# Optimization experiments

Hardware: AMD Instinct MI355X
Metric: run time of the kernel (lower is better)

## Reference

```python
import jax, jax.numpy as jnp
import numpy as np

NUM_DAYS = 4096
NUM_ATTR = 512
MB = 128  # minibatch_size (sliding-window length)
HID = 500


def setup_inputs() -> dict:
    key = jax.random.key(0)
    kx, k1, kb1, k2, kb2 = jax.random.split(key, 5)
    bound1 = 1.0 / np.sqrt(NUM_ATTR)
    bound2 = 1.0 / np.sqrt(HID)
    return {
        "x": jax.random.normal(kx, (NUM_DAYS, NUM_ATTR), dtype=jnp.float32),
        "W1": jax.random.uniform(k1, (NUM_ATTR, HID), jnp.float32, -bound1, bound1),
        "b1": jax.random.uniform(kb1, (HID,), jnp.float32, -bound1, bound1),
        "W2": jax.random.uniform(k2, (HID, 1), jnp.float32, -bound2, bound2),
        "b2": jax.random.uniform(kb2, (1,), jnp.float32, -bound2, bound2),
    }


def reference(x, W1, b1, W2, b2):
    num_days = x.shape[0]
    num_batches = num_days - MB  # number of sliding windows
    # window gather indices: [num_batches, MB]
    idx = jnp.arange(num_batches)[:, None] + jnp.arange(MB)[None, :]
    xw = x[idx]                                   # [num_batches, MB, num_attr]
    h = jnp.einsum('wma,ah->wmh', xw, W1) + b1    # [num_batches, MB, 500]
    out = jnp.einsum('wmh,ho->wmo', h, W2) + b2   # [num_batches, MB, 1]
    # torch loop cats all windows along dim 0 (first window replaces sentinel)
    return out.reshape(num_batches * MB, 1)
```

## Files before the change

### kernel.cpp

```cpp
#include <hip/hip_runtime.h>

#define NUM_DAYS    4096
#define NUM_ATTR    512
#define MB_WIN      128
#define HID         500
#define NUM_BATCHES (NUM_DAYS - MB_WIN)
#define NUM_Y       (NUM_BATCHES + MB_WIN - 1)
#define OUT_ELEMS   (NUM_BATCHES * MB_WIN)

__global__ __launch_bounds__(64) void k_fold_weights(
    const float* __restrict__ W1, const float* __restrict__ b1,
    const float* __restrict__ W2, const float* __restrict__ b2,
    float* __restrict__ v, float* __restrict__ c) {
    const int b    = blockIdx.x;
    const int lane = threadIdx.x;
    const float* src = (b < NUM_ATTR) ? (W1 + (size_t)b * HID) : b1;
    float acc = 0.f;
    const float4* s4 = (const float4*)src;
    const float4* w4 = (const float4*)W2;
    #pragma unroll
    for (int j = lane; j < 125; j += 64) {
        float4 a = s4[j], w = w4[j];
        acc += a.x * w.x + a.y * w.y + a.z * w.z + a.w * w.w;
    }
    #pragma unroll
    for (int off = 32; off >= 1; off >>= 1) acc += __shfl_down(acc, off, 64);
    if (lane == 0) {
        if (b < NUM_ATTR) v[b] = acc;
        else              *c   = acc + b2[0];
    }
}

__global__ __launch_bounds__(64) void k_dot_scatter(
    const float* __restrict__ x, const float* __restrict__ v,
    const float* __restrict__ c, float* __restrict__ out) {
    const int b    = blockIdx.x;
    const int lane = threadIdx.x;
    const int d    = ((b & 15) << 8) | (b >> 4);
    if (d >= NUM_Y) return;

    const float4* xr = (const float4*)(x + (size_t)d * NUM_ATTR);
    const float4* vr = (const float4*)v;
    float4 a0 = xr[lane];
    float4 a1 = xr[lane + 64];
    float4 v0 = vr[lane];
    float4 v1 = vr[lane + 64];
    float acc = a0.x * v0.x + a0.y * v0.y + a0.z * v0.z + a0.w * v0.w
              + a1.x * v1.x + a1.y * v1.y + a1.z * v1.z + a1.w * v1.w;
    #pragma unroll
    for (int off = 32; off >= 1; off >>= 1) acc += __shfl_xor(acc, off, 64);
    const float yv = acc + *c;

    const int m0 = lane,      w0 = d - m0;
    const int m1 = lane + 64, w1 = d - m1;
    if (w0 >= 0 && w0 < NUM_BATCHES) out[(size_t)w0 * MB_WIN + m0] = yv;
    if (w1 >= 0 && w1 < NUM_BATCHES) out[(size_t)w1 * MB_WIN + m1] = yv;
}

extern "C" void kernel_launch(void* const* d_in, const int* in_sizes, int n_in,
                              void* d_out, int out_size, void* d_ws, size_t ws_size,
                              hipStream_t stream) {
    const float* x  = (const float*)d_in[0];
    const float* W1 = (const float*)d_in[1];
    const float* b1 = (const float*)d_in[2];
    const float* W2 = (const float*)d_in[3];
    const float* b2 = (const float*)d_in[4];
    float* out = (float*)d_out;

    float* ws = (float*)d_ws;
    float* v  = ws;
    float* c  = ws + 512;

    k_fold_weights<<<NUM_ATTR + 1, 64, 0, stream>>>(W1, b1, W2, b2, v, c);
    k_dot_scatter<<<NUM_DAYS, 64, 0, stream>>>(x, v, c, out);
}
```

Measured before the change: 69.47 us.

## Split dot-scatter into row dot kernel and coalesced float4 replicate kernel

Splits the fused dot-and-scatter kernel into two. The first computes one scalar per day with four waves per block and writes it to a workspace buffer. The second writes the sliding-window output as contiguous float4 stores that read from the small y buffer. This replaces the strided scattered output writes with fully coalesced vector stores, at the cost of an extra kernel launch and a round trip through the workspace.

```diff
diff --git a/kernel.cpp b/kernel.cpp
--- a/kernel.cpp
+++ b/kernel.cpp
@@ -31,12 +31,12 @@
     }
 }
 
-__global__ __launch_bounds__(64) void k_dot_scatter(
+__global__ __launch_bounds__(256) void k_dot(
     const float* __restrict__ x, const float* __restrict__ v,
-    const float* __restrict__ c, float* __restrict__ out) {
-    const int b    = blockIdx.x;
-    const int lane = threadIdx.x;
-    const int d    = ((b & 15) << 8) | (b >> 4);
+    const float* __restrict__ c, float* __restrict__ y) {
+    const int wv   = threadIdx.x >> 6;
+    const int lane = threadIdx.x & 63;
+    const int d    = (blockIdx.x << 2) | wv;
     if (d >= NUM_Y) return;
 
     const float4* xr = (const float4*)(x + (size_t)d * NUM_ATTR);
@@ -49,12 +49,21 @@
               + a1.x * v1.x + a1.y * v1.y + a1.z * v1.z + a1.w * v1.w;
     #pragma unroll
     for (int off = 32; off >= 1; off >>= 1) acc += __shfl_xor(acc, off, 64);
-    const float yv = acc + *c;
+    if (lane == 0) y[d] = acc + *c;
+}
 
-    const int m0 = lane,      w0 = d - m0;
-    const int m1 = lane + 64, w1 = d - m1;
-    if (w0 >= 0 && w0 < NUM_BATCHES) out[(size_t)w0 * MB_WIN + m0] = yv;
-    if (w1 >= 0 && w1 < NUM_BATCHES) out[(size_t)w1 * MB_WIN + m1] = yv;
+__global__ __launch_bounds__(256) void k_replicate(
+    const float* __restrict__ y, float4* __restrict__ out4) {
+    const int t = blockIdx.x * 256 + threadIdx.x;
+    const int w = t >> 5;
+    const int l = t & 31;
+    const int base = w + (l << 2);
+    float4 r;
+    r.x = y[base + 0];
+    r.y = y[base + 1];
+    r.z = y[base + 2];
+    r.w = y[base + 3];
+    out4[t] = r;
 }
 
 extern "C" void kernel_launch(void* const* d_in, const int* in_sizes, int n_in,
@@ -70,7 +79,9 @@
     float* ws = (float*)d_ws;
     float* v  = ws;
     float* c  = ws + 512;
+    float* y  = ws + 576;
 
     k_fold_weights<<<NUM_ATTR + 1, 64, 0, stream>>>(W1, b1, W2, b2, v, c);
-    k_dot_scatter<<<NUM_DAYS, 64, 0, stream>>>(x, v, c, out);
+    k_dot<<<(NUM_Y + 3) / 4, 256, 0, stream>>>(x, v, c, y);
+    k_replicate<<<(OUT_ELEMS / 4) / 256, 256, 0, stream>>>(y, (float4*)out);
 }
```

Measured after the change: 68.40 us. Within noise of the previous version (-1.5%).

## Compute window dots per output tile in shared memory and write coalesced float4 rows

Applied to the files above, without the earlier changes.

Replaces the per-day dot-and-scatter kernel with one that gives each block 16 output windows. The block recomputes the 143 day dot products those windows need into shared memory, then writes the 16x128 output tile with contiguous float4 stores. This removes the strided scattered writes of the old kernel at the cost of recomputing each x row dot about 9 times, which adds x reads that should mostly hit L2.

```diff
diff --git a/kernel.cpp b/kernel.cpp
--- a/kernel.cpp
+++ b/kernel.cpp
@@ -7,6 +7,9 @@
 #define NUM_BATCHES (NUM_DAYS - MB_WIN)
 #define NUM_Y       (NUM_BATCHES + MB_WIN - 1)
 #define OUT_ELEMS   (NUM_BATCHES * MB_WIN)
+
+#define ROWS_PER_BLK 16
+#define DOTS_PER_BLK (ROWS_PER_BLK + MB_WIN - 1)
 
 __global__ __launch_bounds__(64) void k_fold_weights(
     const float* __restrict__ W1, const float* __restrict__ b1,
@@ -31,30 +34,48 @@
     }
 }
 
-__global__ __launch_bounds__(64) void k_dot_scatter(
+__global__ __launch_bounds__(256) void k_out(
     const float* __restrict__ x, const float* __restrict__ v,
-    const float* __restrict__ c, float* __restrict__ out) {
-    const int b    = blockIdx.x;
-    const int lane = threadIdx.x;
-    const int d    = ((b & 15) << 8) | (b >> 4);
-    if (d >= NUM_Y) return;
+    const float* __restrict__ c, float4* __restrict__ out4) {
+    __shared__ float y_s[DOTS_PER_BLK];
 
-    const float4* xr = (const float4*)(x + (size_t)d * NUM_ATTR);
+    const int wv   = threadIdx.x >> 6;
+    const int lane = threadIdx.x & 63;
+    const int w0   = blockIdx.x * ROWS_PER_BLK;
+
     const float4* vr = (const float4*)v;
-    float4 a0 = xr[lane];
-    float4 a1 = xr[lane + 64];
-    float4 v0 = vr[lane];
-    float4 v1 = vr[lane + 64];
-    float acc = a0.x * v0.x + a0.y * v0.y + a0.z * v0.z + a0.w * v0.w
-              + a1.x * v1.x + a1.y * v1.y + a1.z * v1.z + a1.w * v1.w;
+    const float4  v0 = vr[lane];
+    const float4  v1 = vr[lane + 64];
+    const float   cc = *c;
+
+    for (int i = wv; i < DOTS_PER_BLK; i += 4) {
+        const int d = w0 + i;
+        const float4* xr = (const float4*)(x + (size_t)d * NUM_ATTR);
+        float4 a0 = xr[lane];
+        float4 a1 = xr[lane + 64];
+        float acc = a0.x * v0.x + a0.y * v0.y + a0.z * v0.z + a0.w * v0.w
+                  + a1.x * v1.x + a1.y * v1.y + a1.z * v1.z + a1.w * v1.w;
+        #pragma unroll
+        for (int off = 32; off >= 1; off >>= 1) acc += __shfl_xor(acc, off, 64);
+        if (lane == 0) y_s[i] = acc + cc;
+    }
+
+    __syncthreads();
+
+    const int base4 = w0 * (MB_WIN / 4);
     #pragma unroll
-    for (int off = 32; off >= 1; off >>= 1) acc += __shfl_xor(acc, off, 64);
-    const float yv = acc + *c;
-
-    const int m0 = lane,      w0 = d - m0;
-    const int m1 = lane + 64, w1 = d - m1;
-    if (w0 >= 0 && w0 < NUM_BATCHES) out[(size_t)w0 * MB_WIN + m0] = yv;
-    if (w1 >= 0 && w1 < NUM_BATCHES) out[(size_t)w1 * MB_WIN + m1] = yv;
+    for (int k = 0; k < 2; ++k) {
+        const int t = threadIdx.x + k * 256;
+        const int r = t >> 5;
+        const int l = t & 31;
+        const int s = r + (l << 2);
+        float4 o;
+        o.x = y_s[s + 0];
+        o.y = y_s[s + 1];
+        o.z = y_s[s + 2];
+        o.w = y_s[s + 3];
+        out4[base4 + t] = o;
+    }
 }
 
 extern "C" void kernel_launch(void* const* d_in, const int* in_sizes, int n_in,
@@ -65,12 +86,12 @@
     const float* b1 = (const float*)d_in[2];
     const float* W2 = (const float*)d_in[3];
     const float* b2 = (const float*)d_in[4];
-    float* out = (float*)d_out;
+    float4* out = (float4*)d_out;
 
     float* ws = (float*)d_ws;
     float* v  = ws;
     float* c  = ws + 512;
 
     k_fold_weights<<<NUM_ATTR + 1, 64, 0, stream>>>(W1, b1, W2, b2, v, c);
-    k_dot_scatter<<<NUM_DAYS, 64, 0, stream>>>(x, v, c, out);
+    k_out<<<NUM_BATCHES / ROWS_PER_BLK, 256, 0, stream>>>(x, v, c, out);
 }
```

Measured after the change: 86.58 us. 1.25x slower.
